# Kernel optimization log

Hardware: AMD Instinct MI355X
Metric: run time of the kernel (lower is better)

## Reference

```python
import jax, jax.numpy as jnp
import numpy as np

B, S, H, HID, V, NSPEC = 8, 4096, 1024, 128, 60000, 5
EPS = 1e-12
SLOPE = 0.01  # nn.LeakyReLU default negative_slope


def _leaky(x):
    return jnp.where(x >= 0, x, SLOPE * x)


def setup_inputs() -> dict:
    key = jax.random.key(0)
    ks = jax.random.split(key, 12)
    gene_ids = jax.random.randint(ks[0], (B, S), 0, V)
    cont = jax.random.uniform(ks[1], (B, S), jnp.float32, 0.0, 10.0)
    spec_mask = jax.random.uniform(ks[2], (B, S)) < 0.05
    spec_vals = -jax.random.randint(ks[3], (B, S), 1, NSPEC + 1).astype(jnp.float32)
    expr_values = jnp.where(spec_mask, spec_vals, cont)
    gene_emb = jax.random.normal(ks[4], (V, H), jnp.float32) * 0.02
    W1 = jax.random.normal(ks[5], (HID,), jnp.float32) * 0.5   # Linear(1,128) weight
    b1 = jax.random.normal(ks[6], (HID,), jnp.float32) * 0.1
    W2 = jax.random.normal(ks[7], (HID, H), jnp.float32) * 0.05  # Linear(128,H)
    b2 = jax.random.normal(ks[8], (H,), jnp.float32) * 0.1
    special_emb = jax.random.normal(ks[9], (NSPEC, HID), jnp.float32) * 0.02
    special_emb = special_emb.at[2].set(0.0)  # padding_idx=2
    pos_emb = jax.random.normal(ks[10], (S, H), jnp.float32) * 0.02
    gamma = jnp.ones((H,), jnp.float32)
    beta = jnp.zeros((H,), jnp.float32)
    return dict(gene_ids=gene_ids, expr_values=expr_values, gene_emb=gene_emb,
                W1=W1, b1=b1, W2=W2, b2=b2, special_emb=special_emb,
                pos_emb=pos_emb, gamma=gamma, beta=beta)


def reference(gene_ids, expr_values, gene_emb, W1, b1, W2, b2, special_emb,
              pos_emb, gamma, beta):
    x = expr_values                                  # [B,S]
    special = x < 0                                  # special-token mask
    # mapped special id: -(int(x)+1); clamp so gather is in-range on non-special slots
    mapped = jnp.clip(-(x.astype(jnp.int32) + 1), 0, NSPEC - 1)
    spec_e = special_emb[mapped]                     # [B,S,HID] gather
    cont_e = _leaky(x[..., None] * W1 + b1)          # dense_1 on scalar value
    h = jnp.where(special[..., None], spec_e, cont_e)  # scatter-combine
    expr_e = _leaky(h) @ W2 + b2                     # dense_2 -> [B,S,H]
    emb = gene_emb[gene_ids] + expr_e + pos_emb[None, :, :]
    mu = jnp.mean(emb, axis=-1, keepdims=True)
    var = jnp.mean(jnp.square(emb - mu), axis=-1, keepdims=True)
    out = (emb - mu) * jax.lax.rsqrt(var + EPS) * gamma + beta
    return out  # dropout is identity at inference (p used at train only)
```

## Files before the change

### kernel.cpp

```cpp
#include <hip/hip_runtime.h>
#include <hip/hip_bf16.h>

#define B_DIM   8
#define S_LEN   4096
#define H_DIM   1024
#define HID_DIM 128
#define NSPEC   5
#define NROWS   (HID_DIM + 1 + NSPEC)
#define SLOPE   0.01f
#define LN_EPS  1e-12f
#define NITER   8

typedef float vfloat4 __attribute__((ext_vector_type(4)));

__global__ __launch_bounds__(256) void build_kernel(
        const float* __restrict__ W1,
        const float* __restrict__ b1,
        const float* __restrict__ W2,
        const float* __restrict__ b2,
        const float* __restrict__ spec,
        float* __restrict__ tvals,
        float2* __restrict__ tab) {
    const int row = blockIdx.x;
    const int tid = threadIdx.x;

    __shared__ float tsh[HID_DIM];
    __shared__ float ash[HID_DIM];
    __shared__ float csh[HID_DIM];

    float w = 0.0f, b = 0.0f, t = 0.0f;
    if (tid < HID_DIM) {
        w = W1[tid];
        b = b1[tid];
        t = (w != 0.0f) ? (-b / w) : __builtin_inff();
        tsh[tid] = t;
        if (row == 0) tvals[tid] = t;
    }
    __syncthreads();
    if (tid < HID_DIM) {
        int r = 0;
        #pragma unroll 8
        for (int k2 = 0; k2 < HID_DIM; ++k2) {
            const float t2 = tsh[k2];
            if (t2 < t || (t2 == t && k2 < tid)) ++r;
        }

        float a, c;
        if (row <= HID_DIM) {
            const bool crossed = (r < row);
            bool zpos;
            if (w > 0.0f)      zpos = crossed;
            else if (w < 0.0f) zpos = !crossed;
            else               zpos = (b >= 0.0f);
            const float s = zpos ? 1.0f : (SLOPE * SLOPE);
            a = s * w;
            c = s * b;
        } else {
            const int m = row - (HID_DIM + 1);
            const float e = spec[m * HID_DIM + tid];
            a = 0.0f;
            c = (e >= 0.0f) ? e : SLOPE * e;
        }
        ash[tid] = a;
        csh[tid] = c;
    }
    __syncthreads();

    float4 u = make_float4(0.f, 0.f, 0.f, 0.f);
    float4 v = make_float4(0.f, 0.f, 0.f, 0.f);
    #pragma unroll 4
    for (int k = 0; k < HID_DIM; ++k) {
        const float4 w2 = reinterpret_cast<const float4*>(W2 + (size_t)k * H_DIM)[tid];
        const float a = ash[k], c = csh[k];
        u.x = fmaf(a, w2.x, u.x);  v.x = fmaf(c, w2.x, v.x);
        u.y = fmaf(a, w2.y, u.y);  v.y = fmaf(c, w2.y, v.y);
        u.z = fmaf(a, w2.z, u.z);  v.z = fmaf(c, w2.z, v.z);
        u.w = fmaf(a, w2.w, u.w);  v.w = fmaf(c, w2.w, v.w);
    }
    const float4 bb = reinterpret_cast<const float4*>(b2)[tid];
    float4* trow = reinterpret_cast<float4*>(tab + (size_t)row * H_DIM);
    trow[2 * tid]     = make_float4(u.x, v.x + bb.x, u.y, v.y + bb.y);
    trow[2 * tid + 1] = make_float4(u.z, v.z + bb.z, u.w, v.w + bb.w);
}

__global__ __launch_bounds__(256, 2) void fuse_kernel(
        const int*   __restrict__ gene_ids,
        const float* __restrict__ expr,
        const float* __restrict__ gene_emb,
        const float* __restrict__ pos_emb,
        const float* __restrict__ gamma,
        const float* __restrict__ beta,
        const float* __restrict__ tvals,
        const float2* __restrict__ tab,
        float* __restrict__ out) {
    const int tid  = threadIdx.x;
    const int lane = tid & 63;
    const int w    = blockIdx.x * 4 + (tid >> 6);

    __shared__ float4 gm_lds[H_DIM / 4];
    __shared__ float4 bt_lds[H_DIM / 4];
    gm_lds[tid] = reinterpret_cast<const float4*>(gamma)[tid];
    bt_lds[tid] = reinterpret_cast<const float4*>(beta)[tid];

    const float tka = tvals[lane];
    const float tkb = tvals[lane + 64];
    const float4* pp = reinterpret_cast<const float4*>(pos_emb + (size_t)w * H_DIM);
    float4 p[4];
    #pragma unroll
    for (int q = 0; q < 4; ++q) p[q] = pp[lane + 64 * q];

    __syncthreads();

    float x_c  = expr[w];
    int   gd_c = gene_ids[w];
    float x_n  = expr[w + S_LEN];
    int   gd_n = gene_ids[w + S_LEN];

    float xm_c;
    float4 g_c[4], ta_c[4], tb_c[4];
    {
        const int rc = __popcll(__ballot(tka <= x_c)) + __popcll(__ballot(tkb <= x_c));
        const bool sc = (x_c < 0.0f);
        const int  mc = min(max(-((int)x_c) - 1, 0), NSPEC - 1);
        const int  row = sc ? (HID_DIM + 1 + mc) : rc;
        xm_c = sc ? 0.0f : x_c;
        const float4* gp = reinterpret_cast<const float4*>(gene_emb + (size_t)gd_c * H_DIM);
        const float4* tp = reinterpret_cast<const float4*>(tab + (size_t)row * H_DIM);
        #pragma unroll
        for (int q = 0; q < 4; ++q) {
            const int f = lane + 64 * q;
            g_c[q]  = gp[f];
            ta_c[q] = tp[2 * f];
            tb_c[q] = tp[2 * f + 1];
        }
    }

    #pragma unroll 8
    for (int i = 0; i < NITER; ++i) {
        const int t = w + i * S_LEN;

        float x_n2  = 0.0f;
        int   gd_n2 = 0;
        if (i + 2 < NITER) {
            x_n2  = expr[t + 2 * S_LEN];
            gd_n2 = gene_ids[t + 2 * S_LEN];
        }

        float xm_n = 0.0f;
        float4 g_n[4], ta_n[4], tb_n[4];
        if (i + 1 < NITER) {
            const int rc = __popcll(__ballot(tka <= x_n)) + __popcll(__ballot(tkb <= x_n));
            const bool sn = (x_n < 0.0f);
            const int  mn = min(max(-((int)x_n) - 1, 0), NSPEC - 1);
            const int  rown = sn ? (HID_DIM + 1 + mn) : rc;
            xm_n = sn ? 0.0f : x_n;
            const float4* gp = reinterpret_cast<const float4*>(gene_emb + (size_t)gd_n * H_DIM);
            const float4* tp = reinterpret_cast<const float4*>(tab + (size_t)rown * H_DIM);
            #pragma unroll
            for (int q = 0; q < 4; ++q) {
                const int f = lane + 64 * q;
                g_n[q]  = gp[f];
                ta_n[q] = tp[2 * f];
                tb_n[q] = tp[2 * f + 1];
            }
        }

        float4 e[4];
        float s1 = 0.0f, s2 = 0.0f;
        #pragma unroll
        for (int q = 0; q < 4; ++q) {
            float4 ev;
            ev.x = g_c[q].x + fmaf(xm_c, ta_c[q].x, ta_c[q].y) + p[q].x;
            ev.y = g_c[q].y + fmaf(xm_c, ta_c[q].z, ta_c[q].w) + p[q].y;
            ev.z = g_c[q].z + fmaf(xm_c, tb_c[q].x, tb_c[q].y) + p[q].z;
            ev.w = g_c[q].w + fmaf(xm_c, tb_c[q].z, tb_c[q].w) + p[q].w;
            e[q] = ev;
            s1 += ev.x + ev.y + ev.z + ev.w;
            s2 += ev.x * ev.x + ev.y * ev.y + ev.z * ev.z + ev.w * ev.w;
        }

        #pragma unroll
        for (int off = 32; off >= 1; off >>= 1) {
            s1 += __shfl_xor(s1, off, 64);
            s2 += __shfl_xor(s2, off, 64);
        }

        const float inv  = 1.0f / (float)H_DIM;
        const float mu   = s1 * inv;
        const float rsig = rsqrtf(s2 * inv - mu * mu + LN_EPS);

        vfloat4* op = reinterpret_cast<vfloat4*>(out + (size_t)t * H_DIM);
        #pragma unroll
        for (int q = 0; q < 4; ++q) {
            const int f = lane + 64 * q;
            const float4 gm = gm_lds[f];
            const float4 bt = bt_lds[f];
            vfloat4 o;
            o.x = fmaf((e[q].x - mu) * rsig, gm.x, bt.x);
            o.y = fmaf((e[q].y - mu) * rsig, gm.y, bt.y);
            o.z = fmaf((e[q].z - mu) * rsig, gm.z, bt.z);
            o.w = fmaf((e[q].w - mu) * rsig, gm.w, bt.w);
            __builtin_nontemporal_store(o, op + f);
        }

        xm_c = xm_n;
        x_n  = x_n2;
        gd_n = gd_n2;
        #pragma unroll
        for (int q = 0; q < 4; ++q) {
            g_c[q]  = g_n[q];
            ta_c[q] = ta_n[q];
            tb_c[q] = tb_n[q];
        }
    }
}

extern "C" void kernel_launch(void* const* d_in, const int* in_sizes, int n_in,
                              void* d_out, int out_size, void* d_ws, size_t ws_size,
                              hipStream_t stream) {
    const int*   gene_ids = (const int*)  d_in[0];
    const float* expr     = (const float*)d_in[1];
    const float* gene_emb = (const float*)d_in[2];
    const float* W1       = (const float*)d_in[3];
    const float* b1       = (const float*)d_in[4];
    const float* W2       = (const float*)d_in[5];
    const float* b2       = (const float*)d_in[6];
    const float* spec     = (const float*)d_in[7];
    const float* pos_emb  = (const float*)d_in[8];
    const float* gamma    = (const float*)d_in[9];
    const float* beta     = (const float*)d_in[10];
    float* out = (float*)d_out;

    const size_t tab_bytes = (size_t)NROWS * H_DIM * sizeof(float2);
    float2* tab   = (float2*)d_ws;
    float*  tvals = (float*)((char*)d_ws + tab_bytes);

    const int n_tokens = in_sizes[0];
    const int nwaves   = n_tokens / NITER;

    build_kernel<<<NROWS, 256, 0, stream>>>(W1, b1, W2, b2, spec, tvals, tab);
    fuse_kernel<<<nwaves / 4, 256, 0, stream>>>(gene_ids, expr, gene_emb, pos_emb,
                                                gamma, beta, tvals, tab, out);
}
```

Baseline: 64.75 us.

## Deepen gene-embedding prefetch to two tokens ahead and stage pos_emb in LDS

The gene_emb row gather now runs two tokens ahead of the compute, while the table-row gather stays one token ahead, so the random HBM gather latency is better hidden. To free registers, the per-wave pos_emb row moves from registers into shared memory, and the launch bound occupancy hint rises from 2 to 3 blocks per SIMD/CU. The deeper prefetch adds register pressure and LDS reads each iteration, which could cause spilling or limit occupancy.

```diff
diff --git a/kernel.cpp b/kernel.cpp
--- a/kernel.cpp
+++ b/kernel.cpp
@@ -83,7 +83,7 @@
     trow[2 * tid + 1] = make_float4(u.z, v.z + bb.z, u.w, v.w + bb.w);
 }
 
-__global__ __launch_bounds__(256, 2) void fuse_kernel(
+__global__ __launch_bounds__(256, 3) void fuse_kernel(
         const int*   __restrict__ gene_ids,
         const float* __restrict__ expr,
         const float* __restrict__ gene_emb,
@@ -95,71 +95,94 @@
         float* __restrict__ out) {
     const int tid  = threadIdx.x;
     const int lane = tid & 63;
-    const int w    = blockIdx.x * 4 + (tid >> 6);
+    const int wv   = tid >> 6;
+    const int w    = blockIdx.x * 4 + wv;
 
     __shared__ float4 gm_lds[H_DIM / 4];
     __shared__ float4 bt_lds[H_DIM / 4];
+    __shared__ float4 pos_lds[4][H_DIM / 4];
+
     gm_lds[tid] = reinterpret_cast<const float4*>(gamma)[tid];
     bt_lds[tid] = reinterpret_cast<const float4*>(beta)[tid];
 
     const float tka = tvals[lane];
     const float tkb = tvals[lane + 64];
-    const float4* pp = reinterpret_cast<const float4*>(pos_emb + (size_t)w * H_DIM);
-    float4 p[4];
-    #pragma unroll
-    for (int q = 0; q < 4; ++q) p[q] = pp[lane + 64 * q];
+
+    {
+        const float4* pp = reinterpret_cast<const float4*>(pos_emb + (size_t)w * H_DIM);
+        #pragma unroll
+        for (int q = 0; q < 4; ++q) pos_lds[wv][lane + 64 * q] = pp[lane + 64 * q];
+    }
 
     __syncthreads();
 
-    float x_c  = expr[w];
-    int   gd_c = gene_ids[w];
-    float x_n  = expr[w + S_LEN];
-    int   gd_n = gene_ids[w + S_LEN];
-
+    float x0 = expr[w];
+    int   g0 = gene_ids[w];
+    float x1 = expr[w + S_LEN];
+    int   g1 = gene_ids[w + S_LEN];
+    float x2 = expr[w + 2 * S_LEN];
+    int   g2 = gene_ids[w + 2 * S_LEN];
+
+    float4 g_c[4], g_n1[4], ta_c[4], tb_c[4];
+    {
+        const float4* gpc = reinterpret_cast<const float4*>(gene_emb + (size_t)g0 * H_DIM);
+        const float4* gpn = reinterpret_cast<const float4*>(gene_emb + (size_t)g1 * H_DIM);
+        #pragma unroll
+        for (int q = 0; q < 4; ++q) {
+            const int f = lane + 64 * q;
+            g_c[q]  = gpc[f];
+            g_n1[q] = gpn[f];
+        }
+    }
     float xm_c;
-    float4 g_c[4], ta_c[4], tb_c[4];
     {
-        const int rc = __popcll(__ballot(tka <= x_c)) + __popcll(__ballot(tkb <= x_c));
-        const bool sc = (x_c < 0.0f);
-        const int  mc = min(max(-((int)x_c) - 1, 0), NSPEC - 1);
+        const int rc = __popcll(__ballot(tka <= x0)) + __popcll(__ballot(tkb <= x0));
+        const bool sc = (x0 < 0.0f);
+        const int  mc = min(max(-((int)x0) - 1, 0), NSPEC - 1);
         const int  row = sc ? (HID_DIM + 1 + mc) : rc;
-        xm_c = sc ? 0.0f : x_c;
-        const float4* gp = reinterpret_cast<const float4*>(gene_emb + (size_t)gd_c * H_DIM);
+        xm_c = sc ? 0.0f : x0;
         const float4* tp = reinterpret_cast<const float4*>(tab + (size_t)row * H_DIM);
         #pragma unroll
         for (int q = 0; q < 4; ++q) {
             const int f = lane + 64 * q;
-            g_c[q]  = gp[f];
             ta_c[q] = tp[2 * f];
             tb_c[q] = tp[2 * f + 1];
         }
     }
 
-    #pragma unroll 8
+    float x_a = x1, x_b = x2;
+    int   gid_b = g2;
+
+    #pragma unroll
     for (int i = 0; i < NITER; ++i) {
         const int t = w + i * S_LEN;
 
-        float x_n2  = 0.0f;
-        int   gd_n2 = 0;
+        float x_in = 0.0f;
+        int   gid_in = 0;
+        if (i + 3 < NITER) {
+            x_in   = expr[t + 3 * S_LEN];
+            gid_in = gene_ids[t + 3 * S_LEN];
+        }
+
+        float4 g_n2[4];
         if (i + 2 < NITER) {
-            x_n2  = expr[t + 2 * S_LEN];
-            gd_n2 = gene_ids[t + 2 * S_LEN];
+            const float4* gp = reinterpret_cast<const float4*>(gene_emb + (size_t)gid_b * H_DIM);
+            #pragma unroll
+            for (int q = 0; q < 4; ++q) g_n2[q] = gp[lane + 64 * q];
         }
 
         float xm_n = 0.0f;
-        float4 g_n[4], ta_n[4], tb_n[4];
+        float4 ta_n[4], tb_n[4];
         if (i + 1 < NITER) {
-            const int rc = __popcll(__ballot(tka <= x_n)) + __popcll(__ballot(tkb <= x_n));
-            const bool sn = (x_n < 0.0f);
-            const int  mn = min(max(-((int)x_n) - 1, 0), NSPEC - 1);
+            const int rc = __popcll(__ballot(tka <= x_a)) + __popcll(__ballot(tkb <= x_a));
+            const bool sn = (x_a < 0.0f);
+            const int  mn = min(max(-((int)x_a) - 1, 0), NSPEC - 1);
             const int  rown = sn ? (HID_DIM + 1 + mn) : rc;
-            xm_n = sn ? 0.0f : x_n;
-            const float4* gp = reinterpret_cast<const float4*>(gene_emb + (size_t)gd_n * H_DIM);
+            xm_n = sn ? 0.0f : x_a;
             const float4* tp = reinterpret_cast<const float4*>(tab + (size_t)rown * H_DIM);
             #pragma unroll
             for (int q = 0; q < 4; ++q) {
                 const int f = lane + 64 * q;
-                g_n[q]  = gp[f];
                 ta_n[q] = tp[2 * f];
                 tb_n[q] = tp[2 * f + 1];
             }
@@ -169,11 +192,12 @@
         float s1 = 0.0f, s2 = 0.0f;
         #pragma unroll
         for (int q = 0; q < 4; ++q) {
+            const float4 pq = pos_lds[wv][lane + 64 * q];
             float4 ev;
-            ev.x = g_c[q].x + fmaf(xm_c, ta_c[q].x, ta_c[q].y) + p[q].x;
-            ev.y = g_c[q].y + fmaf(xm_c, ta_c[q].z, ta_c[q].w) + p[q].y;
-            ev.z = g_c[q].z + fmaf(xm_c, tb_c[q].x, tb_c[q].y) + p[q].z;
-            ev.w = g_c[q].w + fmaf(xm_c, tb_c[q].z, tb_c[q].w) + p[q].w;
+            ev.x = g_c[q].x + fmaf(xm_c, ta_c[q].x, ta_c[q].y) + pq.x;
+            ev.y = g_c[q].y + fmaf(xm_c, ta_c[q].z, ta_c[q].w) + pq.y;
+            ev.z = g_c[q].z + fmaf(xm_c, tb_c[q].x, tb_c[q].y) + pq.z;
+            ev.w = g_c[q].w + fmaf(xm_c, tb_c[q].z, tb_c[q].w) + pq.w;
             e[q] = ev;
             s1 += ev.x + ev.y + ev.z + ev.w;
             s2 += ev.x * ev.x + ev.y * ev.y + ev.z * ev.z + ev.w * ev.w;
@@ -203,12 +227,14 @@
             __builtin_nontemporal_store(o, op + f);
         }
 
-        xm_c = xm_n;
-        x_n  = x_n2;
-        gd_n = gd_n2;
-        #pragma unroll
-        for (int q = 0; q < 4; ++q) {
-            g_c[q]  = g_n[q];
+        xm_c  = xm_n;
+        x_a   = x_b;
+        x_b   = x_in;
+        gid_b = gid_in;
+        #pragma unroll
+        for (int q = 0; q < 4; ++q) {
+            g_c[q]  = g_n1[q];
+            g_n1[q] = g_n2[q];
             ta_c[q] = ta_n[q];
             tb_c[q] = tb_n[q];
         }
```

Measured after the change: 85.17 us. +31.5%, slower.
